# Kernel optimization log

Measured on AMD Instinct MI355X. Metric: run time of the kernel, lower is better.

Reference implementation:

```python
import jax, jax.numpy as jnp
import numpy as np

H, DH = 16, 64  # heads, dim_head

def _ln(x, g, b):
    mu = jnp.mean(x, axis=-1, keepdims=True)
    var = jnp.var(x, axis=-1, keepdims=True)
    return (x - mu) * jax.lax.rsqrt(var + 1e-5) * g + b

def setup_inputs() -> dict:
    key = jax.random.key(0)
    ks = jax.random.split(key, 6)
    B, N1, N2, D = 8, 4096, 256, 1024
    inner = H * DH
    x = jax.random.normal(ks[0], (B, N1, D), jnp.float32)
    latents = jax.random.normal(ks[1], (B, N2, D), jnp.float32)
    mask = jnp.ones((B, N1 + N2), jnp.int32)
    Wq = jax.random.normal(ks[2], (D, inner), jnp.float32) / np.float32(np.sqrt(D))
    Wkv = jax.random.normal(ks[3], (D, 2 * inner), jnp.float32) / np.float32(np.sqrt(D))
    Wout = jax.random.normal(ks[4], (inner, D), jnp.float32) / np.float32(np.sqrt(inner))
    g_media = jnp.ones((D,), jnp.float32)
    b_media = jnp.zeros((D,), jnp.float32)
    g_lat = jnp.ones((D,), jnp.float32)
    b_lat = jnp.zeros((D,), jnp.float32)
    return {"x": x, "latents": latents, "mask": mask,
            "g_media": g_media, "b_media": b_media, "g_lat": g_lat, "b_lat": b_lat,
            "Wq": Wq, "Wkv": Wkv, "Wout": Wout}

def reference(x, latents, mask, g_media, b_media, g_lat, b_lat, Wq, Wkv, Wout):
    scale = DH ** -0.5
    xn = _ln(x, g_media, b_media)            # (B, N1, D)
    ln = _ln(latents, g_lat, b_lat)          # (B, N2, D)
    q = ln @ Wq                              # (B, N2, H*DH)
    kv = jnp.concatenate([xn, ln], axis=1) @ Wkv  # (B, N1+N2, 2*H*DH)
    k, v = jnp.split(kv, 2, axis=-1)
    B, N2 = q.shape[0], q.shape[1]
    Nk = k.shape[1]
    q = q.reshape(B, N2, H, DH).transpose(0, 2, 1, 3) * scale  # (B,H,N2,DH)
    k = k.reshape(B, Nk, H, DH).transpose(0, 2, 1, 3)
    v = v.reshape(B, Nk, H, DH).transpose(0, 2, 1, 3)
    sim = jnp.einsum('bhid,bhjd->bhij', q, k)                  # (B,H,N2,Nk)
    sim = sim - jax.lax.stop_gradient(jnp.max(sim, axis=-1, keepdims=True))
    sim = jnp.where(mask[:, None, None, :] == 0, jnp.float32(-10000.0), sim)
    attn = jax.nn.softmax(sim, axis=-1)
    out = jnp.einsum('bhij,bhjd->bhid', attn, v)               # (B,H,N2,DH)
    out = out.transpose(0, 2, 1, 3).reshape(B, N2, H * DH)
    return out @ Wout                                          # (B, N2, D)
```

## Files before the change

kernel.cpp:

```cpp
#include <hip/hip_runtime.h>
#include <stdint.h>

typedef __attribute__((ext_vector_type(4))) float f32x4;
typedef __attribute__((ext_vector_type(4))) int   i32x4;

__device__ __forceinline__ ushort f2bf(float f) {
  union { float f; uint32_t u; } v; v.f = f;
  uint32_t r = v.u + 0x7FFFu + ((v.u >> 16) & 1u);
  return (ushort)(r >> 16);
}
__device__ __forceinline__ void mfma_acc(f32x4& c, i32x4 a, i32x4 b) {
  asm volatile("v_mfma_f32_16x16x32_bf16 %0, %1, %2, %0" : "+v"(c) : "v"(a), "v"(b));
}
__device__ __forceinline__ void gload_lds16(const void* g, void* lds) {
  __builtin_amdgcn_global_load_lds(
      (const __attribute__((address_space(1))) void*)g,
      (__attribute__((address_space(3))) void*)lds, 16, 0, 0);
}

__global__ void __launch_bounds__(256) ln_kernel(
    const float* __restrict__ x, const float* __restrict__ lat,
    const float* __restrict__ gm, const float* __restrict__ bm,
    const float* __restrict__ gl, const float* __restrict__ bl,
    ushort* __restrict__ out) {
  int row = blockIdx.x;
  int b = row / 4352, j = row - b * 4352;
  const float *src, *g, *bi;
  if (j < 4096) { src = x + ((size_t)b * 4096 + j) * 1024; g = gm; bi = bm; }
  else          { src = lat + ((size_t)b * 256 + (j - 4096)) * 1024; g = gl; bi = bl; }
  int t = threadIdx.x;
  f32x4 v = ((const f32x4*)src)[t];
  float s = v.x + v.y + v.z + v.w;
  float q = v.x * v.x + v.y * v.y + v.z * v.z + v.w * v.w;
  #pragma unroll
  for (int o = 1; o < 64; o <<= 1) { s += __shfl_xor(s, o, 64); q += __shfl_xor(q, o, 64); }
  __shared__ float ss[4], sq[4];
  int w = t >> 6, l = t & 63;
  if (l == 0) { ss[w] = s; sq[w] = q; }
  __syncthreads();
  s = ss[0] + ss[1] + ss[2] + ss[3];
  q = sq[0] + sq[1] + sq[2] + sq[3];
  float mu = s * (1.f / 1024.f);
  float var = q * (1.f / 1024.f) - mu * mu;
  float rs = rsqrtf(var + 1e-5f);
  f32x4 gg = ((const f32x4*)g)[t], bb = ((const f32x4*)bi)[t];
  ushort4 o4;
  o4.x = f2bf((v.x - mu) * rs * gg.x + bb.x);
  o4.y = f2bf((v.y - mu) * rs * gg.y + bb.y);
  o4.z = f2bf((v.z - mu) * rs * gg.z + bb.z);
  o4.w = f2bf((v.w - mu) * rs * gg.w + bb.w);
  ((ushort4*)(out + (size_t)row * 1024))[t] = o4;
}

__global__ void __launch_bounds__(256) tsplit3_kernel(
    const float* __restrict__ Wkv, const float* __restrict__ Wq, const float* __restrict__ Wout,
    ushort* __restrict__ wkvt, ushort* __restrict__ wqt, ushort* __restrict__ wot) {
  int bid = blockIdx.x;
  const float* W; ushort* out; int N, bid2;
  if (bid < 1024)      { W = Wkv;  out = wkvt; N = 2048; bid2 = bid; }
  else if (bid < 1536) { W = Wq;   out = wqt;  N = 1024; bid2 = bid - 1024; }
  else                 { W = Wout; out = wot;  N = 1024; bid2 = bid - 1536; }
  int ntn = N >> 6;
  int tk = bid2 / ntn, tn = bid2 - tk * ntn;
  int k0 = tk * 32, n0 = tn * 64;
  __shared__ float tile[32][65];
  int t = threadIdx.x;
  #pragma unroll
  for (int i = 0; i < 8; i++) {
    int idx = t + i * 256;
    int k = idx >> 6, n = idx & 63;
    tile[k][n] = W[(size_t)(k0 + k) * N + n0 + n];
  }
  __syncthreads();
  #pragma unroll
  for (int i = 0; i < 8; i++) {
    int idx = t + i * 256;
    int n = idx >> 5, k = idx & 31;
    out[(size_t)(n0 + n) * 1024 + k0 + k] = f2bf(tile[k][n]);
  }
}

__global__ void __launch_bounds__(512, 2) gemm256_kv(
    const ushort* __restrict__ A, const ushort* __restrict__ Bw,
    ushort* __restrict__ okb, ushort* __restrict__ ovb) {
  int orig = blockIdx.x;
  int bx = (orig & 7) * 136 + (orig >> 3);
  int mt = bx >> 3, nt = bx & 7;
  int m0 = mt * 256, n0 = nt * 256;
  int t = threadIdx.x, w = t >> 6, l = t & 63, lg = l >> 4, lr = l & 15;
  int wr = w >> 2, wc = w & 3;

  __shared__ char smem[131072];

  auto stage = [&](int kt, int bsel) {
    size_t ka = (size_t)kt * 64;
    char* sA = smem + bsel * 65536;
    char* sB = smem + bsel * 65536 + 32768;
    #pragma unroll
    for (int i = 0; i < 4; i++) {
      int c = t + i * 512;
      int row = c >> 3, j = c & 7;
      int sj = j ^ (row & 7);
      gload_lds16(A + ((size_t)(m0 + row) * 1024 + ka + sj * 8), sA + c * 16);
    }
    #pragma unroll
    for (int i = 0; i < 4; i++) {
      int c = t + i * 512;
      int row = c >> 3, j = c & 7;
      int sj = j ^ (row & 7);
      gload_lds16(Bw + ((size_t)(n0 + row) * 1024 + ka + sj * 8), sB + c * 16);
    }
  };

  f32x4 acc[8][4];
  #pragma unroll
  for (int i = 0; i < 8; i++)
    #pragma unroll
    for (int j = 0; j < 4; j++) acc[i][j] = (f32x4){0.f, 0.f, 0.f, 0.f};

  stage(0, 0);
  stage(1, 1);
  const int swz = (lr & 7) << 4;

  for (int kt = 0; kt < 16; kt++) {
    if (kt < 15) asm volatile("s_waitcnt vmcnt(8)" ::: "memory");
    else         asm volatile("s_waitcnt vmcnt(0)" ::: "memory");
    __builtin_amdgcn_s_barrier();
    const char* cA = smem + (kt & 1) * 65536;
    const char* cB = smem + (kt & 1) * 65536 + 32768;
    i32x4 ar[4][2], br[4][2];
    #pragma unroll
    for (int mi = 0; mi < 4; mi++)
      #pragma unroll
      for (int kk = 0; kk < 2; kk++)
        ar[mi][kk] = *(const i32x4*)(cA + ((((wr * 128 + mi * 16 + lr) * 128) + kk * 64 + lg * 16) ^ swz));
    #pragma unroll
    for (int nj = 0; nj < 2; nj++)
      #pragma unroll
      for (int kk = 0; kk < 2; kk++)
        br[nj][kk] = *(const i32x4*)(cB + ((((wc * 64 + nj * 16 + lr) * 128) + kk * 64 + lg * 16) ^ swz));
    __builtin_amdgcn_s_setprio(1);
    #pragma unroll
    for (int mi = 0; mi < 4; mi++)
      #pragma unroll
      for (int nj = 0; nj < 2; nj++)
        #pragma unroll
        for (int kk = 0; kk < 2; kk++) mfma_acc(acc[mi][nj], ar[mi][kk], br[nj][kk]);
    __builtin_amdgcn_s_setprio(0);
    #pragma unroll
    for (int nj = 2; nj < 4; nj++)
      #pragma unroll
      for (int kk = 0; kk < 2; kk++)
        br[nj][kk] = *(const i32x4*)(cB + ((((wc * 64 + nj * 16 + lr) * 128) + kk * 64 + lg * 16) ^ swz));
    __builtin_amdgcn_s_setprio(1);
    #pragma unroll
    for (int mi = 0; mi < 4; mi++)
      #pragma unroll
      for (int nj = 2; nj < 4; nj++)
        #pragma unroll
        for (int kk = 0; kk < 2; kk++) mfma_acc(acc[mi][nj], ar[mi][kk], br[nj][kk]);
    __builtin_amdgcn_s_setprio(0);
    #pragma unroll
    for (int mi = 0; mi < 4; mi++)
      #pragma unroll
      for (int kk = 0; kk < 2; kk++)
        ar[mi][kk] = *(const i32x4*)(cA + ((((wr * 128 + (mi + 4) * 16 + lr) * 128) + kk * 64 + lg * 16) ^ swz));
    __builtin_amdgcn_s_setprio(1);
    #pragma unroll
    for (int mi = 0; mi < 4; mi++)
      #pragma unroll
      for (int nj = 2; nj < 4; nj++)
        #pragma unroll
        for (int kk = 0; kk < 2; kk++) mfma_acc(acc[mi + 4][nj], ar[mi][kk], br[nj][kk]);
    __builtin_amdgcn_s_setprio(0);
    __builtin_amdgcn_s_setprio(1);
    #pragma unroll
    for (int mi = 0; mi < 4; mi++)
      #pragma unroll
      for (int nj = 0; nj < 2; nj++)
        #pragma unroll
        for (int kk = 0; kk < 2; kk++) mfma_acc(acc[mi + 4][nj], ar[mi][kk], br[nj][kk]);
    __builtin_amdgcn_s_setprio(0);
    __builtin_amdgcn_s_barrier();
    if (kt + 2 < 16) stage(kt + 2, kt & 1);
  }

  #pragma unroll
  for (int mi = 0; mi < 8; mi++) {
    #pragma unroll
    for (int r = 0; r < 4; r++) {
      int row = m0 + wr * 128 + mi * 16 + lg * 4 + r;
      int b = row / 4352; int n = row - b * 4352;
      size_t base = (size_t)b * 4456448 + (size_t)n * 64;
      #pragma unroll
      for (int nj = 0; nj < 4; nj++) {
        int col = n0 + wc * 64 + nj * 16 + lr;
        int cc = col & 1023; int h = cc >> 6; int d = cc & 63;
        ushort* dst = (col < 1024) ? okb : ovb;
        dst[base + (size_t)h * 278528 + d] = f2bf(acc[mi][nj][r]);
      }
    }
  }
}

template<int MODE>
__global__ void __launch_bounds__(256, 2) gemm_nt(
    const ushort* __restrict__ A, const ushort* __restrict__ Bw,
    ushort* __restrict__ okb, float* __restrict__ of,
    int ntn, int Keff, int lda, int ldb) {
  int orig = blockIdx.x;
  int bx = ((orig & 7) * (gridDim.x >> 3)) + (orig >> 3);
  int m0 = (bx / ntn) * 128, n0 = (bx - (bx / ntn) * ntn) * 128;
  int t = threadIdx.x, w = t >> 6, l = t & 63, lg = l >> 4, lr = l & 15;
  int wr = w >> 1, wc = w & 1;
  __shared__ ushort As[128 * 32];
  __shared__ ushort Bs[128 * 32];
  f32x4 acc[4][4];
  #pragma unroll
  for (int i = 0; i < 4; i++)
    #pragma unroll
    for (int j = 0; j < 4; j++) acc[i][j] = (f32x4){0.f, 0.f, 0.f, 0.f};

  int nk = Keff >> 5;
  for (int kt = 0; kt < nk; kt++) {
    int ka = kt * 32;
    #pragma unroll
    for (int c2 = 0; c2 < 2; c2++) {
      int c = w * 2 + c2;
      int arow = m0 + c * 16 + (l >> 2);
      if (MODE == 1) arow = ((arow >> 8) * 4352) + 4096 + (arow & 255);
      gload_lds16(A + (size_t)arow * lda + ka + (l & 3) * 8, &As[c * 512]);
    }
    #pragma unroll
    for (int c2 = 0; c2 < 2; c2++) {
      int c = w * 2 + c2;
      int brow = n0 + c * 16 + (l >> 2);
      gload_lds16(Bw + (size_t)brow * ldb + ka + (l & 3) * 8, &Bs[c * 512]);
    }
    __syncthreads();
    i32x4 af[4], bf[4];
    #pragma unroll
    for (int mi = 0; mi < 4; mi++)
      af[mi] = *(const i32x4*)&As[(wr * 64 + mi * 16 + lr) * 32 + lg * 8];
    #pragma unroll
    for (int nj = 0; nj < 4; nj++)
      bf[nj] = *(const i32x4*)&Bs[(wc * 64 + nj * 16 + lr) * 32 + lg * 8];
    #pragma unroll
    for (int mi = 0; mi < 4; mi++)
      #pragma unroll
      for (int nj = 0; nj < 4; nj++) mfma_acc(acc[mi][nj], af[mi], bf[nj]);
    __syncthreads();
  }

  #pragma unroll
  for (int mi = 0; mi < 4; mi++) {
    #pragma unroll
    for (int r = 0; r < 4; r++) {
      int row = m0 + wr * 64 + mi * 16 + lg * 4 + r;
      if (MODE == 1) {
        int b = row >> 8; int n2 = row & 255;
        size_t base = (size_t)b * 262144 + (size_t)n2 * 64;
        #pragma unroll
        for (int nj = 0; nj < 4; nj++) {
          int col = n0 + wc * 64 + nj * 16 + lr;
          int h = col >> 6; int d = col & 63;
          okb[base + (size_t)h * 16384 + d] = f2bf(acc[mi][nj][r] * 0.125f);
        }
      } else {
        #pragma unroll
        for (int nj = 0; nj < 4; nj++) {
          int col = n0 + wc * 64 + nj * 16 + lr;
          of[(size_t)row * 1024 + col] = acc[mi][nj][r];
        }
      }
    }
  }
}

__global__ void __launch_bounds__(256) vtrans_kernel(const ushort* __restrict__ v,
                                                     ushort* __restrict__ vt) {
  int bh = blockIdx.x / 68, tk = blockIdx.x - bh * 68;
  __shared__ ushort tl[64][65];
  int t = threadIdx.x;
  const ushort* src = v + (size_t)bh * 278528 + (size_t)tk * 4096;
  #pragma unroll
  for (int c2 = 0; c2 < 2; c2++) {
    int idx = t + c2 * 256;
    int row = idx >> 3, cb = idx & 7;
    i32x4 d4 = *(const i32x4*)(src + row * 64 + cb * 8);
    const ushort* p = (const ushort*)&d4;
    #pragma unroll
    for (int e = 0; e < 8; e++) tl[row][cb * 8 + e] = p[e];
  }
  __syncthreads();
  ushort* dst = vt + (size_t)bh * 278528 + tk * 64;
  #pragma unroll
  for (int i = 0; i < 16; i++) {
    int idx = t + i * 256;
    int d = idx >> 6, key = idx & 63;
    dst[(size_t)d * 4352 + key] = tl[key][d];
  }
}

__global__ void __launch_bounds__(256, 2) attn_kernel(
    const ushort* __restrict__ qb, const ushort* __restrict__ kb,
    const ushort* __restrict__ vt, const int* __restrict__ mask,
    ushort* __restrict__ ao) {
  int orig = blockIdx.x;
  int bid = ((orig & 7) << 6) + (orig >> 3);
  int qt = bid & 3; int h = (bid >> 2) & 15; int b = bid >> 6;
  int t = threadIdx.x, w = t >> 6, l = t & 63, lg = l >> 4, lr = l & 15;
  __shared__ ushort Kl[2][4096];
  __shared__ ushort Vl[2][4096];
  __shared__ ushort Pl[64 * 72];
  __shared__ float bias[4352];
  size_t bh = (size_t)b * 16 + h;
  const ushort* qhead = qb + bh * 16384 + (size_t)qt * 4096;
  const ushort* khead = kb + bh * 278528;
  const ushort* vthead = vt + bh * 278528;

  #pragma unroll
  for (int c2 = 0; c2 < 2; c2++) {
    int c = w * 2 + c2;
    int row = c * 8 + (l >> 3);
    int colb = ((l & 7) * 16) ^ ((row & 7) << 4);
    gload_lds16((const char*)qhead + row * 128 + colb, (char*)Kl + c * 1024);
  }
  for (int i = t; i < 4352; i += 256)
    bias[i] = mask[b * 4352 + i] ? -24.0f : -10024.0f;
  __syncthreads();
  i32x4 aq[2];
  #pragma unroll
  for (int kh = 0; kh < 2; kh++) {
    int row = w * 16 + lr;
    int off = (row * 128 + kh * 64 + lg * 16) ^ ((row & 7) << 4);
    aq[kh] = *(const i32x4*)((const char*)Kl + off);
  }
  __syncthreads();

  auto stage = [&](int tk, int bsel) {
    #pragma unroll
    for (int c2 = 0; c2 < 2; c2++) {
      int c = w * 2 + c2;
      int row = c * 8 + (l >> 3);
      int colb = ((l & 7) * 16) ^ ((row & 7) << 4);
      gload_lds16((const char*)khead + (size_t)(tk * 64 + row) * 128 + colb,
                  (char*)Kl + bsel * 8192 + c * 1024);
      gload_lds16((const char*)vthead + (size_t)row * 8704 + (size_t)tk * 128 + colb,
                  (char*)Vl + bsel * 8192 + c * 1024);
    }
  };

  float lsum[4];
  f32x4 oacc[4];
  #pragma unroll
  for (int r = 0; r < 4; r++) lsum[r] = 0.f;
  #pragma unroll
  for (int df = 0; df < 4; df++) oacc[df] = (f32x4){0.f, 0.f, 0.f, 0.f};

  stage(0, 0);
  int cur = 0;
  for (int tk = 0; tk < 68; tk++) {
    if (tk < 67) {
      stage(tk + 1, cur ^ 1);
      asm volatile("s_waitcnt vmcnt(4)" ::: "memory");
    } else {
      asm volatile("s_waitcnt vmcnt(0)" ::: "memory");
    }
    asm volatile("s_barrier" ::: "memory");
    const char* Kb = (const char*)Kl + cur * 8192;
    const char* Vb = (const char*)Vl + cur * 8192;

    f32x4 sf[4];
    #pragma unroll
    for (int kf = 0; kf < 4; kf++) {
      f32x4 s = (f32x4){0.f, 0.f, 0.f, 0.f};
      #pragma unroll
      for (int kh = 0; kh < 2; kh++) {
        int row = kf * 16 + lr;
        int off = (row * 128 + kh * 64 + lg * 16) ^ ((row & 7) << 4);
        i32x4 bk = *(const i32x4*)(Kb + off);
        mfma_acc(s, aq[kh], bk);
      }
      sf[kf] = s;
    }
    #pragma unroll
    for (int kf = 0; kf < 4; kf++) {
      float ma = bias[tk * 64 + kf * 16 + lr];
      #pragma unroll
      for (int r = 0; r < 4; r++) {
        float p = __expf(sf[kf][r] + ma);
        lsum[r] += p;
        Pl[(w * 16 + lg * 4 + r) * 72 + kf * 16 + lr] = f2bf(p);
      }
    }
    #pragma unroll
    for (int kq = 0; kq < 2; kq++) {
      i32x4 ap = *(const i32x4*)&Pl[(w * 16 + lr) * 72 + kq * 32 + lg * 8];
      #pragma unroll
      for (int df = 0; df < 4; df++) {
        int row = df * 16 + lr;
        int off = (row * 128 + kq * 64 + lg * 16) ^ ((row & 7) << 4);
        i32x4 bv = *(const i32x4*)(Vb + off);
        mfma_acc(oacc[df], ap, bv);
      }
    }
    asm volatile("s_barrier" ::: "memory");
    cur ^= 1;
  }
  #pragma unroll
  for (int o = 1; o < 16; o <<= 1)
    #pragma unroll
    for (int r = 0; r < 4; r++) lsum[r] += __shfl_xor(lsum[r], o, 64);
  #pragma unroll
  for (int r = 0; r < 4; r++) lsum[r] = 1.f / lsum[r];
  int n2 = qt * 64 + w * 16 + lg * 4;
  #pragma unroll
  for (int df = 0; df < 4; df++)
    #pragma unroll
    for (int r = 0; r < 4; r++) {
      float vv = oacc[df][r] * lsum[r];
      ao[((size_t)b * 256 + (n2 + r)) * 1024 + h * 64 + df * 16 + lr] = f2bf(vv);
    }
}

extern "C" void kernel_launch(void* const* d_in, const int* in_sizes, int n_in,
                              void* d_out, int out_size, void* d_ws, size_t ws_size,
                              hipStream_t stream) {
  const float* x    = (const float*)d_in[0];
  const float* lat  = (const float*)d_in[1];
  const int*   msk  = (const int*)d_in[2];
  const float* gm   = (const float*)d_in[3];
  const float* bm   = (const float*)d_in[4];
  const float* gl   = (const float*)d_in[5];
  const float* bl   = (const float*)d_in[6];
  const float* Wq   = (const float*)d_in[7];
  const float* Wkv  = (const float*)d_in[8];
  const float* Wout = (const float*)d_in[9];
  float* out = (float*)d_out;
  char* ws = (char*)d_ws;

  ushort* xcat  = (ushort*)(ws);
  ushort* kbuf  = (ushort*)(ws + 71303168);
  ushort* vbuf  = (ushort*)(ws + 142606336);
  ushort* qbuf  = (ushort*)(ws + 213909504);
  ushort* aobuf = (ushort*)(ws + 218103808);
  ushort* wkvt  = (ushort*)(ws + 222298112);
  ushort* wqt   = (ushort*)(ws + 226492416);
  ushort* wot   = (ushort*)(ws + 228589568);
  ushort* vt    = xcat;

  ln_kernel<<<34816, 256, 0, stream>>>(x, lat, gm, bm, gl, bl, xcat);
  tsplit3_kernel<<<2048, 256, 0, stream>>>(Wkv, Wq, Wout, wkvt, wqt, wot);
  gemm256_kv<<<1088, 512, 0, stream>>>(xcat, wkvt, kbuf, vbuf);
  gemm_nt<1><<<16 * 8, 256, 0, stream>>>(xcat, wqt, qbuf, nullptr, 8, 1024, 1024, 1024);
  vtrans_kernel<<<128 * 68, 256, 0, stream>>>(vbuf, vt);
  attn_kernel<<<512, 256, 0, stream>>>(qbuf, kbuf, vt, msk, aobuf);
  gemm_nt<2><<<16 * 8, 256, 0, stream>>>(aobuf, wot, nullptr, out, 8, 1024, 1024, 1024);
}
```

Before: 373.9 us.

## Restructure KV GEMM into four quadrant sub-tiles with staggered half-tile prefetch

The 256x256 KV projection GEMM now splits each K-step into four 128x128 quadrant products, with each wave owning a 64x32 piece of every quadrant. Loads of the next K-tile are issued per 128-row half as soon as that half's LDS buffer has been consumed, instead of one bulk prefetch after the whole step. The goal is to interleave global-to-LDS traffic with MFMA work more finely and smooth the memory pipeline. In exchange it adds more barriers per K-step and more complex buffer reuse, where an ordering mistake could corrupt data.

```diff
diff --git a/kernel.cpp b/kernel.cpp
--- a/kernel.cpp
+++ b/kernel.cpp
@@ -92,112 +92,147 @@
 
   __shared__ char smem[131072];
 
-  auto stage = [&](int kt, int bsel) {
-    size_t ka = (size_t)kt * 64;
-    char* sA = smem + bsel * 65536;
-    char* sB = smem + bsel * 65536 + 32768;
-    #pragma unroll
-    for (int i = 0; i < 4; i++) {
+  auto stageH = [&](const ushort* src, int rowbase, int h, int T, char* dst) {
+    #pragma unroll
+    for (int i = 0; i < 2; i++) {
       int c = t + i * 512;
-      int row = c >> 3, j = c & 7;
-      int sj = j ^ (row & 7);
-      gload_lds16(A + ((size_t)(m0 + row) * 1024 + ka + sj * 8), sA + c * 16);
-    }
-    #pragma unroll
-    for (int i = 0; i < 4; i++) {
-      int c = t + i * 512;
-      int row = c >> 3, j = c & 7;
-      int sj = j ^ (row & 7);
-      gload_lds16(Bw + ((size_t)(n0 + row) * 1024 + ka + sj * 8), sB + c * 16);
+      int rl = c >> 3, j = c & 7;
+      int sj = j ^ (rl & 7);
+      gload_lds16(src + ((size_t)(rowbase + h * 128 + rl) * 1024 + (size_t)T * 64 + sj * 8),
+                  dst + c * 16);
     }
   };
 
-  f32x4 acc[8][4];
-  #pragma unroll
-  for (int i = 0; i < 8; i++)
-    #pragma unroll
-    for (int j = 0; j < 4; j++) acc[i][j] = (f32x4){0.f, 0.f, 0.f, 0.f};
-
-  stage(0, 0);
-  stage(1, 1);
-  const int swz = (lr & 7) << 4;
-
-  for (int kt = 0; kt < 16; kt++) {
-    if (kt < 15) asm volatile("s_waitcnt vmcnt(8)" ::: "memory");
-    else         asm volatile("s_waitcnt vmcnt(0)" ::: "memory");
-    __builtin_amdgcn_s_barrier();
-    const char* cA = smem + (kt & 1) * 65536;
-    const char* cB = smem + (kt & 1) * 65536 + 32768;
-    i32x4 ar[4][2], br[4][2];
-    #pragma unroll
-    for (int mi = 0; mi < 4; mi++)
+  f32x4 acc[4][4][2];
+  #pragma unroll
+  for (int p = 0; p < 4; p++)
+    #pragma unroll
+    for (int i = 0; i < 4; i++)
+      #pragma unroll
+      for (int j = 0; j < 2; j++) acc[p][i][j] = (f32x4){0.f, 0.f, 0.f, 0.f};
+
+  stageH(A,  m0, 0, 0, smem);
+  stageH(A,  m0, 1, 0, smem + 16384);
+  stageH(Bw, n0, 0, 0, smem + 32768);
+  stageH(Bw, n0, 1, 0, smem + 49152);
+  stageH(A,  m0, 0, 1, smem + 65536);
+  stageH(Bw, n0, 1, 1, smem + 65536 + 49152);
+  asm volatile("s_waitcnt vmcnt(4)" ::: "memory");
+  __builtin_amdgcn_s_barrier();
+
+  const int arl = wr * 64 + lr;
+  const int brl = wc * 32 + lr;
+  const int kcol0 = lg * 16;
+
+  for (int T = 0; T < 16; T++) {
+    char* cs = smem + (T & 1) * 65536;
+    char* ns = smem + ((T + 1) & 1) * 65536;
+    i32x4 a[4][2], b[2][2];
+
+    #pragma unroll
+    for (int mi = 0; mi < 4; mi++) {
+      int rl = arl + mi * 16;
       #pragma unroll
       for (int kk = 0; kk < 2; kk++)
-        ar[mi][kk] = *(const i32x4*)(cA + ((((wr * 128 + mi * 16 + lr) * 128) + kk * 64 + lg * 16) ^ swz));
-    #pragma unroll
-    for (int nj = 0; nj < 2; nj++)
+        a[mi][kk] = *(const i32x4*)(cs + rl * 128 + ((kk * 64 + kcol0) ^ ((rl & 7) << 4)));
+    }
+    #pragma unroll
+    for (int nj = 0; nj < 2; nj++) {
+      int rl = brl + nj * 16;
       #pragma unroll
       for (int kk = 0; kk < 2; kk++)
-        br[nj][kk] = *(const i32x4*)(cB + ((((wc * 64 + nj * 16 + lr) * 128) + kk * 64 + lg * 16) ^ swz));
+        b[nj][kk] = *(const i32x4*)(cs + 32768 + rl * 128 + ((kk * 64 + kcol0) ^ ((rl & 7) << 4)));
+    }
+    if (T + 1 < 16) stageH(A, m0, 1, T + 1, ns + 16384);
+    __builtin_amdgcn_s_barrier();
     __builtin_amdgcn_s_setprio(1);
     #pragma unroll
     for (int mi = 0; mi < 4; mi++)
       #pragma unroll
       for (int nj = 0; nj < 2; nj++)
         #pragma unroll
-        for (int kk = 0; kk < 2; kk++) mfma_acc(acc[mi][nj], ar[mi][kk], br[nj][kk]);
+        for (int kk = 0; kk < 2; kk++) mfma_acc(acc[0][mi][nj], a[mi][kk], b[nj][kk]);
     __builtin_amdgcn_s_setprio(0);
-    #pragma unroll
-    for (int nj = 2; nj < 4; nj++)
+    __builtin_amdgcn_s_barrier();
+
+    #pragma unroll
+    for (int nj = 0; nj < 2; nj++) {
+      int rl = brl + nj * 16;
       #pragma unroll
       for (int kk = 0; kk < 2; kk++)
-        br[nj][kk] = *(const i32x4*)(cB + ((((wc * 64 + nj * 16 + lr) * 128) + kk * 64 + lg * 16) ^ swz));
+        b[nj][kk] = *(const i32x4*)(cs + 49152 + rl * 128 + ((kk * 64 + kcol0) ^ ((rl & 7) << 4)));
+    }
+    if (T + 1 < 16) stageH(Bw, n0, 0, T + 1, ns + 32768);
+    __builtin_amdgcn_s_barrier();
     __builtin_amdgcn_s_setprio(1);
     #pragma unroll
     for (int mi = 0; mi < 4; mi++)
       #pragma unroll
-      for (int nj = 2; nj < 4; nj++)
-        #pragma unroll
-        for (int kk = 0; kk < 2; kk++) mfma_acc(acc[mi][nj], ar[mi][kk], br[nj][kk]);
+      for (int nj = 0; nj < 2; nj++)
+        #pragma unroll
+        for (int kk = 0; kk < 2; kk++) mfma_acc(acc[1][mi][nj], a[mi][kk], b[nj][kk]);
     __builtin_amdgcn_s_setprio(0);
-    #pragma unroll
-    for (int mi = 0; mi < 4; mi++)
+    __builtin_amdgcn_s_barrier();
+
+    #pragma unroll
+    for (int mi = 0; mi < 4; mi++) {
+      int rl = arl + mi * 16;
       #pragma unroll
       for (int kk = 0; kk < 2; kk++)
-        ar[mi][kk] = *(const i32x4*)(cA + ((((wr * 128 + (mi + 4) * 16 + lr) * 128) + kk * 64 + lg * 16) ^ swz));
+        a[mi][kk] = *(const i32x4*)(cs + 16384 + rl * 128 + ((kk * 64 + kcol0) ^ ((rl & 7) << 4)));
+    }
+    if (T + 2 < 16) stageH(A, m0, 0, T + 2, cs);
+    __builtin_amdgcn_s_barrier();
     __builtin_amdgcn_s_setprio(1);
     #pragma unroll
     for (int mi = 0; mi < 4; mi++)
       #pragma unroll
-      for (int nj = 2; nj < 4; nj++)
-        #pragma unroll
-        for (int kk = 0; kk < 2; kk++) mfma_acc(acc[mi + 4][nj], ar[mi][kk], br[nj][kk]);
+      for (int nj = 0; nj < 2; nj++)
+        #pragma unroll
+        for (int kk = 0; kk < 2; kk++) mfma_acc(acc[2][mi][nj], a[mi][kk], b[nj][kk]);
     __builtin_amdgcn_s_setprio(0);
+    __builtin_amdgcn_s_barrier();
+
+    #pragma unroll
+    for (int nj = 0; nj < 2; nj++) {
+      int rl = brl + nj * 16;
+      #pragma unroll
+      for (int kk = 0; kk < 2; kk++)
+        b[nj][kk] = *(const i32x4*)(cs + 32768 + rl * 128 + ((kk * 64 + kcol0) ^ ((rl & 7) << 4)));
+    }
+    if (T + 2 < 16) stageH(Bw, n0, 1, T + 2, cs + 49152);
+    __builtin_amdgcn_s_barrier();
     __builtin_amdgcn_s_setprio(1);
     #pragma unroll
     for (int mi = 0; mi < 4; mi++)
       #pragma unroll
       for (int nj = 0; nj < 2; nj++)
         #pragma unroll
-        for (int kk = 0; kk < 2; kk++) mfma_acc(acc[mi + 4][nj], ar[mi][kk], br[nj][kk]);
+        for (int kk = 0; kk < 2; kk++) mfma_acc(acc[3][mi][nj], a[mi][kk], b[nj][kk]);
     __builtin_amdgcn_s_setprio(0);
-    __builtin_amdgcn_s_barrier();
-    if (kt + 2 < 16) stage(kt + 2, kt & 1);
-  }
-
-  #pragma unroll
-  for (int mi = 0; mi < 8; mi++) {
-    #pragma unroll
-    for (int r = 0; r < 4; r++) {
-      int row = m0 + wr * 128 + mi * 16 + lg * 4 + r;
-      int b = row / 4352; int n = row - b * 4352;
-      size_t base = (size_t)b * 4456448 + (size_t)n * 64;
-      #pragma unroll
-      for (int nj = 0; nj < 4; nj++) {
-        int col = n0 + wc * 64 + nj * 16 + lr;
-        int cc = col & 1023; int h = cc >> 6; int d = cc & 63;
-        ushort* dst = (col < 1024) ? okb : ovb;
-        dst[base + (size_t)h * 278528 + d] = f2bf(acc[mi][nj][r]);
+    if (T < 14) asm volatile("s_waitcnt vmcnt(4)" ::: "memory");
+    else        asm volatile("s_waitcnt vmcnt(0)" ::: "memory");
+    __builtin_amdgcn_s_barrier();
+  }
+
+  const int qmt[4] = {0, 0, 1, 1};
+  const int qnt[4] = {0, 1, 1, 0};
+  #pragma unroll
+  for (int p = 0; p < 4; p++) {
+    #pragma unroll
+    for (int mi = 0; mi < 4; mi++) {
+      #pragma unroll
+      for (int r = 0; r < 4; r++) {
+        int row = m0 + qmt[p] * 128 + wr * 64 + mi * 16 + lg * 4 + r;
+        int bb = row / 4352; int n = row - bb * 4352;
+        size_t base = (size_t)bb * 4456448 + (size_t)n * 64;
+        #pragma unroll
+        for (int nj = 0; nj < 2; nj++) {
+          int col = n0 + qnt[p] * 128 + wc * 32 + nj * 16 + lr;
+          int cc = col & 1023; int h = cc >> 6; int d = cc & 63;
+          ushort* dst = (col < 1024) ? okb : ovb;
+          dst[base + (size_t)h * 278528 + d] = f2bf(acc[p][mi][nj][r]);
+        }
       }
     }
   }
```

After: 363.8 us. 1.03x faster.
